# Performance work log

Hardware: AMD Instinct MI355X
Metric: run time of the kernel (lower is better)

## Reference

```python
import jax, jax.numpy as jnp
import numpy as np

B, N, C, H, TR = 2, 5000, 256, 8, 2
M = N // TR  # reduced KV length from Conv1d(data_len, data_len//tr, 1)
DK = C // H


def setup_inputs() -> dict:
    key = jax.random.key(0)
    ks = jax.random.split(key, 10)
    s = 0.02
    return {
        "x": jax.random.normal(ks[0], (B, N, C), jnp.float32),
        "Wq": jax.random.normal(ks[1], (C, C), jnp.float32) * s,
        "bq": jnp.zeros((C,), jnp.float32),
        "Wk": jax.random.normal(ks[2], (C, C), jnp.float32) * s,
        "bk": jnp.zeros((C,), jnp.float32),
        "Wv": jax.random.normal(ks[3], (C, C), jnp.float32) * s,
        "bv": jnp.zeros((C,), jnp.float32),
        "Wc": jax.random.normal(ks[4], (M, N), jnp.float32) * (1.0 / np.sqrt(N)),
        "bc": jnp.zeros((M,), jnp.float32),
        "gamma": jnp.ones((C,), jnp.float32),
        "beta": jnp.zeros((C,), jnp.float32),
    }


def _layernorm(x, gamma, beta, eps=1e-5):
    mu = jnp.mean(x, axis=-1, keepdims=True)
    var = jnp.mean(jnp.square(x - mu), axis=-1, keepdims=True)
    return gamma * (x - mu) * jax.lax.rsqrt(var + eps) + beta


def reference(x, Wq, bq, Wk, bk, Wv, bv, Wc, bc, gamma, beta):
    b, n, c = x.shape
    # Q projection: (B, H, N, DK)
    q = (x @ Wq.T + bq).reshape(b, n, H, DK).transpose(0, 2, 1, 3)
    # Spatial reduction: Conv1d with kernel size 1 over the N (channel) dim,
    # then LayerNorm over feature dim C
    x_ = jnp.einsum('mn,bnc->bmc', Wc, x) + bc[None, :, None]
    x_ = _layernorm(x_, gamma, beta)
    k = (x_ @ Wk.T + bk).reshape(b, -1, H, DK).transpose(0, 2, 1, 3)  # (B,H,M,DK)
    v = (x_ @ Wv.T + bv).reshape(b, -1, H, DK).transpose(0, 2, 1, 3)  # (B,H,M,DK)
    # Naive attention (full score matrix, as in the original module)
    scores = jnp.einsum('bhnd,bhmd->bhnm', q, k) / jnp.sqrt(jnp.asarray(DK, x.dtype))
    p = jax.nn.softmax(scores, axis=-1)
    out = jnp.einsum('bhnm,bhmd->bhnd', p, v)
    # note: output_linear is declared in __init__ but never applied in forward
    return out.transpose(0, 2, 1, 3).reshape(b, n, c)
```

## Files before the change

kernel.cpp:

```cpp
#include <hip/hip_runtime.h>
#include <hip/hip_bf16.h>
#include <hip/hip_fp16.h>
#include <math.h>

constexpr int B = 2;
constexpr int N = 5000;
constexpr int C = 256;
constexpr int H = 8;
constexpr int DK = 32;
constexpr int M = 2500;
constexpr int MP = 2512;
constexpr int KSTEPS = 157;
constexpr int SPLIT = 8;
constexpr int MTILES = 79;
constexpr float QSCALE = 0.2550598692503365f;

typedef __attribute__((ext_vector_type(8))) short bf16x8;
typedef __attribute__((ext_vector_type(4))) float f32x4;

static __device__ __forceinline__ ushort f2bf(float f) {
  __hip_bfloat16 h = __float2bfloat16(f);
  return *reinterpret_cast<ushort*>(&h);
}

static __device__ __forceinline__ float fastexp2(float x) {
#if __has_builtin(__builtin_amdgcn_exp2f)
  return __builtin_amdgcn_exp2f(x);
#else
  return exp2f(x);
#endif
}

__global__ __launch_bounds__(256) void wcast(const float* __restrict__ Wq,
                                             const float* __restrict__ Wk,
                                             const float* __restrict__ Wv,
                                             ushort* __restrict__ W16) {
  const float* src = (blockIdx.y == 0) ? Wq : (blockIdx.y == 1) ? Wk : Wv;
  const int idx = blockIdx.x * 1024 + threadIdx.x * 4;
  const float4 v = *reinterpret_cast<const float4*>(src + idx);
  ushort4 o;
  o.x = f2bf(v.x); o.y = f2bf(v.y); o.z = f2bf(v.z); o.w = f2bf(v.w);
  *reinterpret_cast<ushort4*>(W16 + (size_t)blockIdx.y * C * C + idx) = o;
}

__global__ __launch_bounds__(256) void xt_cast(const float* __restrict__ x,
                                               ushort* __restrict__ xTt,
                                               ushort* __restrict__ xb16) {
  const int n0 = blockIdx.x * 64, c0 = blockIdx.y * 64, b = blockIdx.z;
  const int tid = threadIdx.x;
  __shared__ ushort T[64][68];
  const float* xb = x + (size_t)b * N * C;
#pragma unroll
  for (int i = 0; i < 4; ++i) {
    const int nl = (tid >> 4) + i * 16;
    const int cg = (tid & 15) * 4;
    float4 v = {0.f, 0.f, 0.f, 0.f};
    const bool ok = (n0 + nl) < N;
    if (ok) v = *reinterpret_cast<const float4*>(xb + (size_t)(n0 + nl) * C + c0 + cg);
    ushort4 u;
    u.x = f2bf(v.x); u.y = f2bf(v.y); u.z = f2bf(v.z); u.w = f2bf(v.w);
    T[nl][cg + 0] = u.x; T[nl][cg + 1] = u.y; T[nl][cg + 2] = u.z; T[nl][cg + 3] = u.w;
    if (ok)
      *reinterpret_cast<ushort4*>(xb16 + ((size_t)b * N + n0 + nl) * C + c0 + cg) = u;
  }
  __syncthreads();
  ushort* ob = xTt + (size_t)b * KSTEPS * C * 32;
  const int cl = tid & 63, ng = tid >> 6;
#pragma unroll
  for (int j = 0; j < 2; ++j) {
    const int nstart = ng * 16 + j * 8;
    const int n = n0 + nstart;
    if (n >= KSTEPS * 32) continue;
    const int ks = n >> 5, kk = n & 31;
    ushort vals[8];
#pragma unroll
    for (int jj = 0; jj < 8; ++jj) vals[jj] = T[nstart + jj][cl];
    *reinterpret_cast<bf16x8*>(ob + ((size_t)ks * C + (c0 + cl)) * 32 + kk) =
        *reinterpret_cast<const bf16x8*>(vals);
  }
}

__global__ __launch_bounds__(256) void conv_mfma(const float* __restrict__ Wc,
                                                 const ushort* __restrict__ xTt,
                                                 ushort* __restrict__ xpart) {
  const int s = blockIdx.x & 7;
  const int mt = blockIdx.x >> 3;
  const int m0 = mt * 32;
  const int tid = threadIdx.x, w = tid >> 6, l = tid & 63;
  const int lr = l & 15, lg = l >> 4;
  f32x4 acc[16];
#pragma unroll
  for (int i = 0; i < 16; ++i) acc[i] = (f32x4){0.f, 0.f, 0.f, 0.f};
  const int row0 = m0 + lr, row1 = m0 + 16 + lr;
  const bool ok0 = row0 < M, ok1 = row1 < M;
  const float* ap0 = Wc + (size_t)(ok0 ? row0 : 0) * N + lg * 8;
  const float* ap1 = Wc + (size_t)(ok1 ? row1 : 0) * N + lg * 8;
  const int crow = w * 64 + lr;

#pragma unroll 2
  for (int ks = s; ks < KSTEPS; ks += SPLIT) {
    const int n0 = ks * 32;
    const bool kok = (n0 + lg * 8) < N;
    bf16x8 a0 = {0, 0, 0, 0, 0, 0, 0, 0}, a1 = {0, 0, 0, 0, 0, 0, 0, 0};
    if (ok0 && kok) {
      const float4 v0 = *reinterpret_cast<const float4*>(ap0 + n0);
      const float4 v1 = *reinterpret_cast<const float4*>(ap0 + n0 + 4);
      ushort u[8];
      u[0] = f2bf(v0.x); u[1] = f2bf(v0.y); u[2] = f2bf(v0.z); u[3] = f2bf(v0.w);
      u[4] = f2bf(v1.x); u[5] = f2bf(v1.y); u[6] = f2bf(v1.z); u[7] = f2bf(v1.w);
      a0 = *reinterpret_cast<const bf16x8*>(u);
    }
    if (ok1 && kok) {
      const float4 v0 = *reinterpret_cast<const float4*>(ap1 + n0);
      const float4 v1 = *reinterpret_cast<const float4*>(ap1 + n0 + 4);
      ushort u[8];
      u[0] = f2bf(v0.x); u[1] = f2bf(v0.y); u[2] = f2bf(v0.z); u[3] = f2bf(v0.w);
      u[4] = f2bf(v1.x); u[5] = f2bf(v1.y); u[6] = f2bf(v1.z); u[7] = f2bf(v1.w);
      a1 = *reinterpret_cast<const bf16x8*>(u);
    }
    bf16x8 bf[8];
#pragma unroll
    for (int ct = 0; ct < 4; ++ct)
#pragma unroll
      for (int bb = 0; bb < 2; ++bb)
        bf[ct * 2 + bb] = *reinterpret_cast<const bf16x8*>(
            xTt + (((size_t)bb * KSTEPS + ks) * C + crow + ct * 16) * 32 + lg * 8);
#pragma unroll
    for (int ct = 0; ct < 4; ++ct)
#pragma unroll
      for (int bb = 0; bb < 2; ++bb) {
        acc[(0 * 4 + ct) * 2 + bb] =
            __builtin_amdgcn_mfma_f32_16x16x32_bf16(a0, bf[ct * 2 + bb], acc[(0 * 4 + ct) * 2 + bb], 0, 0, 0);
        acc[(1 * 4 + ct) * 2 + bb] =
            __builtin_amdgcn_mfma_f32_16x16x32_bf16(a1, bf[ct * 2 + bb], acc[(1 * 4 + ct) * 2 + bb], 0, 0, 0);
      }
  }

#pragma unroll
  for (int mf = 0; mf < 2; ++mf)
#pragma unroll
    for (int ct = 0; ct < 4; ++ct)
#pragma unroll
      for (int bb = 0; bb < 2; ++bb)
#pragma unroll
        for (int i = 0; i < 4; ++i) {
          const int m = m0 + mf * 16 + lg * 4 + i;
          if (m < M) {
            const __half hv = __float2half(acc[(mf * 4 + ct) * 2 + bb][i]);
            xpart[(((size_t)s * B + bb) * M + m) * C + w * 64 + ct * 16 + lr] =
                *reinterpret_cast<const ushort*>(&hv);
          }
        }
}

__global__ __launch_bounds__(256) void ln_kernel(const ushort* __restrict__ xp,
                                                 const float* __restrict__ bc,
                                                 const float* __restrict__ gamma,
                                                 const float* __restrict__ beta,
                                                 ushort* __restrict__ xr16) {
  const int row = blockIdx.x;
  const int tid = threadIdx.x;
  const int b = row / M, m = row - b * M;
  const size_t base = (size_t)row * C;
  float v = bc[m];
#pragma unroll
  for (int s = 0; s < SPLIT; ++s) {
    const ushort us = xp[(((size_t)s * B + b) * M + m) * C + tid];
    v += __half2float(*reinterpret_cast<const __half*>(&us));
  }
  __shared__ float red[8];
  float sum = v;
#pragma unroll
  for (int o = 32; o >= 1; o >>= 1) sum += __shfl_xor(sum, o);
  if ((tid & 63) == 0) red[tid >> 6] = sum;
  __syncthreads();
  const float mu = (red[0] + red[1] + red[2] + red[3]) * (1.f / C);
  const float d = v - mu;
  float s2 = d * d;
#pragma unroll
  for (int o = 32; o >= 1; o >>= 1) s2 += __shfl_xor(s2, o);
  if ((tid & 63) == 0) red[4 + (tid >> 6)] = s2;
  __syncthreads();
  const float var = (red[4] + red[5] + red[6] + red[7]) * (1.f / C);
  xr16[base + tid] = f2bf(gamma[tid] * d * rsqrtf(var + 1e-5f) + beta[tid]);
}

__global__ __launch_bounds__(256) void proj_all(const ushort* __restrict__ xb16,
                                                const ushort* __restrict__ xr16,
                                                const ushort* __restrict__ W16,
                                                const float* __restrict__ bq,
                                                const float* __restrict__ bk,
                                                const float* __restrict__ bv,
                                                ushort* __restrict__ qb,
                                                ushort* __restrict__ kb,
                                                ushort* __restrict__ vt) {
  const int z = blockIdx.z;
  const int R = (z == 0) ? N : M;
  const int totalRows = B * R;
  if (blockIdx.x * 64 >= totalRows) return;
  const ushort* xin = (z == 0) ? xb16 : xr16;
  const ushort* W = W16 + (size_t)z * C * C;
  const float* bias = (z == 0) ? bq : (z == 1) ? bk : bv;
  const int tid = threadIdx.x, w = tid >> 6, l = tid & 63;
  const int lr = l & 15, lg = l >> 4;
  const int r0 = blockIdx.x * 64 + w * 16;
  const int c0 = blockIdx.y * 64;
  const int arow = r0 + lr;
  const bool aok = arow < totalRows;
  f32x4 acc[4] = {{0.f,0.f,0.f,0.f},{0.f,0.f,0.f,0.f},{0.f,0.f,0.f,0.f},{0.f,0.f,0.f,0.f}};
#pragma unroll
  for (int ks = 0; ks < 8; ++ks) {
    bf16x8 af = {0, 0, 0, 0, 0, 0, 0, 0};
    if (aok) af = *reinterpret_cast<const bf16x8*>(xin + (size_t)arow * C + ks * 32 + lg * 8);
#pragma unroll
    for (int ct = 0; ct < 4; ++ct) {
      const bf16x8 bf =
          *reinterpret_cast<const bf16x8*>(W + (size_t)(c0 + ct * 16 + lr) * C + ks * 32 + lg * 8);
      acc[ct] = __builtin_amdgcn_mfma_f32_16x16x32_bf16(af, bf, acc[ct], 0, 0, 0);
    }
  }
#pragma unroll
  for (int ct = 0; ct < 4; ++ct) {
    const int c = c0 + ct * 16 + lr;
    const int h = c >> 5, d = c & 31;
    const float bi = bias[c];
#pragma unroll
    for (int i = 0; i < 4; ++i) {
      const int row = r0 + lg * 4 + i;
      if (row >= totalRows) continue;
      const int bb = (row >= R) ? 1 : 0;
      const int rr = row - bb * R;
      float val = acc[ct][i] + bi;
      if (z == 0) {
        val *= QSCALE;
        qb[(((size_t)bb * H + h) * N + rr) * DK + d] = f2bf(val);
      } else if (z == 1) {
        kb[(((size_t)bb * H + h) * M + rr) * DK + d] = f2bf(val);
      } else {
        vt[(((size_t)bb * H + h) * DK + d) * MP + rr] = f2bf(val);
      }
    }
  }
}

__global__ __launch_bounds__(256) void attn12(const ushort* __restrict__ q,
                                              const ushort* __restrict__ kk,
                                              const ushort* __restrict__ vt,
                                              float* __restrict__ o0,
                                              float* __restrict__ o1,
                                              float* __restrict__ ps0,
                                              float* __restrict__ ps1) {
  const int qt = blockIdx.x, h = blockIdx.y, z = blockIdx.z;
  const int b = z >> 1, half = z & 1;
  const int tid = threadIdx.x, w = tid >> 6, l = tid & 63;
  const int lr = l & 15, lg = l >> 4;
  const int n0 = qt * 256 + w * 64;
  __shared__ ushort Plds[4][2][16][72];
  const ushort* qp = q + (size_t)(b * H + h) * N * DK;
  const ushort* kp = kk + (size_t)(b * H + h) * M * DK;
  const ushort* vp = vt + (size_t)(b * H + h) * DK * MP;
  float* op = half ? o1 : o0;
  float* ps = half ? ps1 : ps0;

  bf16x8 qf[4];
#pragma unroll
  for (int f = 0; f < 4; ++f) {
    const int row = n0 + f * 16 + lr;
    qf[f] = (bf16x8){0, 0, 0, 0, 0, 0, 0, 0};
    if (row < N) qf[f] = *reinterpret_cast<const bf16x8*>(qp + (size_t)row * DK + lg * 8);
  }

  f32x4 O[8];
#pragma unroll
  for (int i = 0; i < 8; ++i) O[i] = (f32x4){0.f, 0.f, 0.f, 0.f};
  float psr[4] = {0.f, 0.f, 0.f, 0.f};

  const int tbeg = half ? 20 : 0;
  const int tend = half ? 40 : 20;
#pragma unroll 1
  for (int t = tbeg; t < tend; ++t) {
    const int m0 = t * 64;
    const bool full = (m0 + 64) <= M;
    bf16x8 kf[4];
#pragma unroll
    for (int ct = 0; ct < 4; ++ct) {
      const int mr = m0 + ct * 16 + lr;
      if (full || mr < M)
        kf[ct] = *reinterpret_cast<const bf16x8*>(kp + (size_t)mr * DK + lg * 8);
      else
        kf[ct] = (bf16x8){0, 0, 0, 0, 0, 0, 0, 0};
    }
    bf16x8 vf[4];
#pragma unroll
    for (int dt = 0; dt < 2; ++dt) {
      const ushort* vb = vp + (size_t)(dt * 16 + lr) * MP + m0 + lg * 8;
      vf[dt * 2 + 0] = *reinterpret_cast<const bf16x8*>(vb);
      vf[dt * 2 + 1] = *reinterpret_cast<const bf16x8*>(vb + 32);
    }
#pragma unroll
    for (int pr = 0; pr < 2; ++pr) {
      const int f0 = pr * 2, f1 = pr * 2 + 1;
#pragma unroll
      for (int ct = 0; ct < 4; ++ct) {
        const f32x4 s0 = __builtin_amdgcn_mfma_f32_16x16x32_bf16(
            kf[ct], qf[f0], (f32x4){0.f, 0.f, 0.f, 0.f}, 0, 0, 0);
        const f32x4 s1 = __builtin_amdgcn_mfma_f32_16x16x32_bf16(
            kf[ct], qf[f1], (f32x4){0.f, 0.f, 0.f, 0.f}, 0, 0, 0);
        float p0[4], p1[4];
#pragma unroll
        for (int i = 0; i < 4; ++i) {
          const bool mok = full || (m0 + ct * 16 + lg * 4 + i) < M;
          p0[i] = mok ? fastexp2(s0[i]) : 0.f;
          p1[i] = mok ? fastexp2(s1[i]) : 0.f;
          psr[f0] += p0[i];
          psr[f1] += p1[i];
        }
        __hip_bfloat162 a01 = __float22bfloat162_rn(make_float2(p0[0], p0[1]));
        __hip_bfloat162 a23 = __float22bfloat162_rn(make_float2(p0[2], p0[3]));
        uint2 u0;
        u0.x = *reinterpret_cast<unsigned*>(&a01);
        u0.y = *reinterpret_cast<unsigned*>(&a23);
        *reinterpret_cast<uint2*>(&Plds[w][0][lr][ct * 16 + lg * 4]) = u0;
        __hip_bfloat162 b01 = __float22bfloat162_rn(make_float2(p1[0], p1[1]));
        __hip_bfloat162 b23 = __float22bfloat162_rn(make_float2(p1[2], p1[3]));
        uint2 u1;
        u1.x = *reinterpret_cast<unsigned*>(&b01);
        u1.y = *reinterpret_cast<unsigned*>(&b23);
        *reinterpret_cast<uint2*>(&Plds[w][1][lr][ct * 16 + lg * 4]) = u1;
      }
      const bf16x8 pa00 = *reinterpret_cast<const bf16x8*>(&Plds[w][0][lr][lg * 8]);
      const bf16x8 pa01 = *reinterpret_cast<const bf16x8*>(&Plds[w][0][lr][32 + lg * 8]);
      const bf16x8 pa10 = *reinterpret_cast<const bf16x8*>(&Plds[w][1][lr][lg * 8]);
      const bf16x8 pa11 = *reinterpret_cast<const bf16x8*>(&Plds[w][1][lr][32 + lg * 8]);
#pragma unroll
      for (int dt = 0; dt < 2; ++dt) {
        O[f0 * 2 + dt] =
            __builtin_amdgcn_mfma_f32_16x16x32_bf16(pa00, vf[dt * 2 + 0], O[f0 * 2 + dt], 0, 0, 0);
        O[f0 * 2 + dt] =
            __builtin_amdgcn_mfma_f32_16x16x32_bf16(pa01, vf[dt * 2 + 1], O[f0 * 2 + dt], 0, 0, 0);
        O[f1 * 2 + dt] =
            __builtin_amdgcn_mfma_f32_16x16x32_bf16(pa10, vf[dt * 2 + 0], O[f1 * 2 + dt], 0, 0, 0);
        O[f1 * 2 + dt] =
            __builtin_amdgcn_mfma_f32_16x16x32_bf16(pa11, vf[dt * 2 + 1], O[f1 * 2 + dt], 0, 0, 0);
      }
    }
  }

#pragma unroll
  for (int f = 0; f < 4; ++f) {
    psr[f] += __shfl_xor(psr[f], 16);
    psr[f] += __shfl_xor(psr[f], 32);
  }
  if (lg == 0) {
    const size_t pbase = ((size_t)b * H + h) * N;
#pragma unroll
    for (int f = 0; f < 4; ++f) {
      const int row = n0 + f * 16 + lr;
      if (row < N) ps[pbase + row] = psr[f];
    }
  }
#pragma unroll
  for (int f = 0; f < 4; ++f)
#pragma unroll
    for (int i = 0; i < 4; ++i) {
      const int row = n0 + f * 16 + lg * 4 + i;
      if (row >= N) continue;
      float* ob = op + ((size_t)b * N + row) * C + h * DK + lr;
      ob[0] = O[f * 2 + 0][i];
      ob[16] = O[f * 2 + 1][i];
    }
}

__global__ __launch_bounds__(256) void attn_combine(float* __restrict__ out,
                                                    const float* __restrict__ o1,
                                                    const float* __restrict__ ps0,
                                                    const float* __restrict__ ps1) {
  const int row = blockIdx.x;
  const int c = threadIdx.x;
  const int b = row / N, n = row - b * N;
  const size_t pidx = ((size_t)b * H + (c >> 5)) * N + n;
  const float denom = ps0[pidx] + ps1[pidx];
  const size_t idx = (size_t)row * C + c;
  out[idx] = (out[idx] + o1[idx]) / denom;
}

extern "C" void kernel_launch(void* const* d_in, const int* in_sizes, int n_in,
                              void* d_out, int out_size, void* d_ws, size_t ws_size,
                              hipStream_t stream) {
  (void)in_sizes; (void)n_in; (void)out_size; (void)ws_size;
  const float* x     = (const float*)d_in[0];
  const float* Wq    = (const float*)d_in[1];
  const float* bq    = (const float*)d_in[2];
  const float* Wk    = (const float*)d_in[3];
  const float* bk    = (const float*)d_in[4];
  const float* Wv    = (const float*)d_in[5];
  const float* bv    = (const float*)d_in[6];
  const float* Wc    = (const float*)d_in[7];
  const float* bc    = (const float*)d_in[8];
  const float* gamma = (const float*)d_in[9];
  const float* beta  = (const float*)d_in[10];
  float* out = (float*)d_out;

  char* wsb = (char*)d_ws;
  ushort* xpart = (ushort*)wsb;
  ushort* qb = (ushort*)wsb;
  ushort* kb = (ushort*)(wsb + 5120000);
  ushort* vt = (ushort*)(wsb + 7680000);
  float* ps0 = (float*)(wsb + 10400000);
  float* ps1 = (float*)(wsb + 10720000);
  char* p = wsb + 20480000;
  ushort* xTt  = (ushort*)p;
  ushort* xr16 = (ushort*)p;
  float* o1 = (float*)p;
  p += 5144576;
  ushort* xb16 = (ushort*)p; p += 5120000;
  ushort* W16  = (ushort*)p;

  wcast<<<dim3(64, 3), 256, 0, stream>>>(Wq, Wk, Wv, W16);
  xt_cast<<<dim3((N + 63) / 64, C / 64, B), 256, 0, stream>>>(x, xTt, xb16);
  conv_mfma<<<dim3(MTILES * SPLIT), 256, 0, stream>>>(Wc, xTt, xpart);
  ln_kernel<<<dim3(B * M), 256, 0, stream>>>(xpart, bc, gamma, beta, xr16);
  (void)hipMemsetAsync(vt, 0, (size_t)B * H * DK * MP * 2 + 4096, stream);
  proj_all<<<dim3((B * N + 63) / 64, C / 64, 3), 256, 0, stream>>>(xb16, xr16, W16, bq, bk, bv,
                                                                   qb, kb, vt);
  attn12<<<dim3((N + 255) / 256, H, B * 2), 256, 0, stream>>>(qb, kb, vt, out, o1, ps0, ps1);
  attn_combine<<<dim3(B * N), 256, 0, stream>>>(out, o1, ps0, ps1);
}
```

Measured before the change: 176.1 us.

## Split attention KV range four ways when workspace allows, vectorize combine

Result: faster. 171.5 us (median of 2 runs) (-2.6%).

```diff
diff --git a/kernel.cpp b/kernel.cpp
--- a/kernel.cpp
+++ b/kernel.cpp
@@ -248,10 +248,12 @@
                                               const ushort* __restrict__ vt,
                                               float* __restrict__ o0,
                                               float* __restrict__ o1,
-                                              float* __restrict__ ps0,
-                                              float* __restrict__ ps1) {
+                                              float* __restrict__ o2,
+                                              float* __restrict__ o3,
+                                              float* __restrict__ psb,
+                                              int nspl, int tilesPer) {
   const int qt = blockIdx.x, h = blockIdx.y, z = blockIdx.z;
-  const int b = z >> 1, half = z & 1;
+  const int b = z / nspl, half = z - b * nspl;
   const int tid = threadIdx.x, w = tid >> 6, l = tid & 63;
   const int lr = l & 15, lg = l >> 4;
   const int n0 = qt * 256 + w * 64;
@@ -259,8 +261,8 @@
   const ushort* qp = q + (size_t)(b * H + h) * N * DK;
   const ushort* kp = kk + (size_t)(b * H + h) * M * DK;
   const ushort* vp = vt + (size_t)(b * H + h) * DK * MP;
-  float* op = half ? o1 : o0;
-  float* ps = half ? ps1 : ps0;
+  float* op = (half == 0) ? o0 : (half == 1) ? o1 : (half == 2) ? o2 : o3;
+  float* ps = psb + (size_t)half * B * H * N;
 
   bf16x8 qf[4];
 #pragma unroll
@@ -275,8 +277,8 @@
   for (int i = 0; i < 8; ++i) O[i] = (f32x4){0.f, 0.f, 0.f, 0.f};
   float psr[4] = {0.f, 0.f, 0.f, 0.f};
 
-  const int tbeg = half ? 20 : 0;
-  const int tend = half ? 40 : 20;
+  const int tbeg = half * tilesPer;
+  const int tend = tbeg + tilesPer;
 #pragma unroll 1
   for (int t = tbeg; t < tend; ++t) {
     const int m0 = t * 64;
@@ -373,21 +375,39 @@
 
 __global__ __launch_bounds__(256) void attn_combine(float* __restrict__ out,
                                                     const float* __restrict__ o1,
-                                                    const float* __restrict__ ps0,
-                                                    const float* __restrict__ ps1) {
-  const int row = blockIdx.x;
-  const int c = threadIdx.x;
-  const int b = row / N, n = row - b * N;
-  const size_t pidx = ((size_t)b * H + (c >> 5)) * N + n;
-  const float denom = ps0[pidx] + ps1[pidx];
-  const size_t idx = (size_t)row * C + c;
-  out[idx] = (out[idx] + o1[idx]) / denom;
+                                                    const float* __restrict__ o2,
+                                                    const float* __restrict__ o3,
+                                                    const float* __restrict__ psb,
+                                                    int nspl) {
+  const int total4 = B * N * C / 4;
+  const size_t psStride = (size_t)B * H * N;
+  for (int i4 = blockIdx.x * 256 + threadIdx.x; i4 < total4; i4 += gridDim.x * 256) {
+    const size_t f = (size_t)i4 * 4;
+    const int row = (int)(f / C);
+    const int c = (int)(f - (size_t)row * C);
+    const int b = row / N, n = row - b * N;
+    const size_t pidx = ((size_t)b * H + (c >> 5)) * N + n;
+    float denom = psb[pidx] + psb[psStride + pidx];
+    float4 acc = *reinterpret_cast<const float4*>(out + f);
+    const float4 v1 = *reinterpret_cast<const float4*>(o1 + f);
+    acc.x += v1.x; acc.y += v1.y; acc.z += v1.z; acc.w += v1.w;
+    if (nspl == 4) {
+      denom += psb[2 * psStride + pidx] + psb[3 * psStride + pidx];
+      const float4 v2 = *reinterpret_cast<const float4*>(o2 + f);
+      const float4 v3 = *reinterpret_cast<const float4*>(o3 + f);
+      acc.x += v2.x + v3.x; acc.y += v2.y + v3.y;
+      acc.z += v2.z + v3.z; acc.w += v2.w + v3.w;
+    }
+    const float inv = 1.f / denom;
+    acc.x *= inv; acc.y *= inv; acc.z *= inv; acc.w *= inv;
+    *reinterpret_cast<float4*>(out + f) = acc;
+  }
 }
 
 extern "C" void kernel_launch(void* const* d_in, const int* in_sizes, int n_in,
                               void* d_out, int out_size, void* d_ws, size_t ws_size,
                               hipStream_t stream) {
-  (void)in_sizes; (void)n_in; (void)out_size; (void)ws_size;
+  (void)in_sizes; (void)n_in; (void)out_size;
   const float* x     = (const float*)d_in[0];
   const float* Wq    = (const float*)d_in[1];
   const float* bq    = (const float*)d_in[2];
@@ -401,20 +421,30 @@
   const float* beta  = (const float*)d_in[10];
   float* out = (float*)d_out;
 
+  constexpr size_t OSZ = (size_t)B * N * C * 4;
+  const int nspl = (ws_size >= 42400000) ? 4 : 2;
+  const int tilesPer = 40 / nspl;
+
   char* wsb = (char*)d_ws;
   ushort* xpart = (ushort*)wsb;
   ushort* qb = (ushort*)wsb;
   ushort* kb = (ushort*)(wsb + 5120000);
   ushort* vt = (ushort*)(wsb + 7680000);
-  float* ps0 = (float*)(wsb + 10400000);
-  float* ps1 = (float*)(wsb + 10720000);
+  float* psb = (float*)(wsb + 10400000);
   char* p = wsb + 20480000;
   ushort* xTt  = (ushort*)p;
   ushort* xr16 = (ushort*)p;
-  float* o1 = (float*)p;
   p += 5144576;
   ushort* xb16 = (ushort*)p; p += 5120000;
   ushort* W16  = (ushort*)p;
+  float *o1, *o2 = nullptr, *o3 = nullptr;
+  if (nspl == 4) {
+    o1 = (float*)(wsb + 11680000);
+    o2 = (float*)(wsb + 11680000 + OSZ);
+    o3 = (float*)(wsb + 11680000 + 2 * OSZ);
+  } else {
+    o1 = (float*)(wsb + 20480000);
+  }
 
   wcast<<<dim3(64, 3), 256, 0, stream>>>(Wq, Wk, Wv, W16);
   xt_cast<<<dim3((N + 63) / 64, C / 64, B), 256, 0, stream>>>(x, xTt, xb16);
@@ -423,6 +453,7 @@
   (void)hipMemsetAsync(vt, 0, (size_t)B * H * DK * MP * 2 + 4096, stream);
   proj_all<<<dim3((B * N + 63) / 64, C / 64, 3), 256, 0, stream>>>(xb16, xr16, W16, bq, bk, bv,
                                                                    qb, kb, vt);
-  attn12<<<dim3((N + 255) / 256, H, B * 2), 256, 0, stream>>>(qb, kb, vt, out, o1, ps0, ps1);
-  attn_combine<<<dim3(B * N), 256, 0, stream>>>(out, o1, ps0, ps1);
-}
+  attn12<<<dim3((N + 255) / 256, H, B * nspl), 256, 0, stream>>>(qb, kb, vt, out, o1, o2, o3,
+                                                                 psb, nspl, tilesPer);
+  attn_combine<<<dim3(1600), 256, 0, stream>>>(out, o1, o2, o3, psb, nspl);
+}
```
